# Kernel tuning notes

Hardware: AMD Instinct MI355X
Metric: run time of the kernel (lower is better)

## Reference

```python
import jax, jax.numpy as jnp
import numpy as np

N_NODES = 100000


def _sage_layer(x, src, dst, Wl, Wr, b):
    # mean-aggregate source features at destination nodes
    msgs = x[src]                                                # [E, d_in]
    agg = jax.ops.segment_sum(msgs, dst, num_segments=N_NODES)  # [N, d_in]
    cnt = jax.ops.segment_sum(jnp.ones((src.shape[0], 1), x.dtype), dst,
                              num_segments=N_NODES)             # [N, 1]
    mean = agg / jnp.maximum(cnt, 1.0)
    # PyG SAGEConv: lin_l(aggr) + lin_r(x); lin_l carries the bias
    return mean @ Wl.T + x @ Wr.T + b


def setup_inputs() -> dict:
    key = jax.random.key(0)
    ks = jax.random.split(key, 9)
    d_in, d_h, d_out, E = 128, 128, 64, 1600000
    s = 1.0 / np.sqrt(d_in)
    inp = {
        "x": jax.random.normal(ks[0], (N_NODES, d_in), jnp.float32),
        "Wl0": jax.random.normal(ks[1], (d_h, d_in), jnp.float32) * s,
        "Wr0": jax.random.normal(ks[2], (d_h, d_in), jnp.float32) * s,
        "b0": jnp.zeros((d_h,), jnp.float32),
        "Wl1": jax.random.normal(ks[3], (d_h, d_h), jnp.float32) * s,
        "Wr1": jax.random.normal(ks[4], (d_h, d_h), jnp.float32) * s,
        "b1": jnp.zeros((d_h,), jnp.float32),
        "Wl2": jax.random.normal(ks[5], (d_out, d_h), jnp.float32) * s,
        "Wr2": jax.random.normal(ks[6], (d_out, d_h), jnp.float32) * s,
        "b2": jnp.zeros((d_out,), jnp.float32),
        "edge_index": jax.random.randint(ks[7], (2, E), 0, N_NODES, jnp.int64),
    }
    return inp


def reference(x, Wl0, Wr0, b0, Wl1, Wr1, b1, Wl2, Wr2, b2, edge_index):
    src, dst = edge_index[0], edge_index[1]
    h = jax.nn.relu(_sage_layer(x, src, dst, Wl0, Wr0, b0))  # dropout = identity (eval)
    h = jax.nn.relu(_sage_layer(h, src, dst, Wl1, Wr1, b1))
    return _sage_layer(h, src, dst, Wl2, Wr2, b2)
```

## Files before the change

kernel.cpp:

```cpp
#include <hip/hip_runtime.h>

#define D 128
typedef unsigned short u16;
typedef unsigned int u32;
typedef __attribute__((ext_vector_type(8))) short short8;
typedef __attribute__((ext_vector_type(16))) float float16;

__device__ __forceinline__ u16 f2bf(float f) {
    u32 u = __builtin_bit_cast(u32, f);
    u += 0x7FFFu + ((u >> 16) & 1u);
    return (u16)(u >> 16);
}
__device__ __forceinline__ float bf2f(u16 b) {
    return __builtin_bit_cast(float, ((u32)b) << 16);
}
__device__ __forceinline__ short8 zero8() {
    short8 z;
    #pragma unroll
    for (int i = 0; i < 8; ++i) z[i] = 0;
    return z;
}


__global__ __launch_bounds__(256) void hist_kernel(const int* __restrict__ dst,
                                                   int* __restrict__ cnt, int E) {
    int e = blockIdx.x * 256 + threadIdx.x;
    if (e < E) atomicAdd(&cnt[dst[e]], 1);
}

__global__ __launch_bounds__(256) void scan1_kernel(const int* __restrict__ cnt,
        int* __restrict__ rowptr, int* __restrict__ blksum, int N) {
    __shared__ int sdata[256];
    const int base = blockIdx.x * 1024 + threadIdx.x * 4;
    int v0 = 0, v1 = 0, v2 = 0, v3 = 0;
    if (base + 3 < N) {
        int4 q = *reinterpret_cast<const int4*>(cnt + base);
        v0 = q.x; v1 = q.y; v2 = q.z; v3 = q.w;
    } else {
        if (base + 0 < N) v0 = cnt[base + 0];
        if (base + 1 < N) v1 = cnt[base + 1];
        if (base + 2 < N) v2 = cnt[base + 2];
    }
    const int t = v0 + v1 + v2 + v3;
    int val = t;
    sdata[threadIdx.x] = val;
    __syncthreads();
    for (int off = 1; off < 256; off <<= 1) {
        int other = (threadIdx.x >= off) ? sdata[threadIdx.x - off] : 0;
        __syncthreads();
        val += other;
        sdata[threadIdx.x] = val;
        __syncthreads();
    }
    const int excl = val - t;
    if (base + 0 < N) rowptr[base + 0] = excl;
    if (base + 1 < N) rowptr[base + 1] = excl + v0;
    if (base + 2 < N) rowptr[base + 2] = excl + v0 + v1;
    if (base + 3 < N) rowptr[base + 3] = excl + v0 + v1 + v2;
    if (threadIdx.x == 255) blksum[blockIdx.x] = val;
}

__global__ __launch_bounds__(256) void scan2_kernel(int* __restrict__ blksum, int nb) {
    __shared__ int s[256];
    const int t = threadIdx.x;
    const int v = (t < nb) ? blksum[t] : 0;
    int val = v;
    s[t] = val;
    __syncthreads();
    for (int off = 1; off < 256; off <<= 1) {
        int o = (t >= off) ? s[t - off] : 0;
        __syncthreads();
        val += o;
        s[t] = val;
        __syncthreads();
    }
    if (t < nb) blksum[t] = val - v;
    if (t == 255) blksum[nb] = val;
}

__global__ __launch_bounds__(256) void scan3_kernel(int* __restrict__ rowptr,
        const int* __restrict__ blksum, int N) {
    const int base = blockIdx.x * 1024 + threadIdx.x * 4;
    const int off = blksum[blockIdx.x];
    #pragma unroll
    for (int k = 0; k < 4; ++k)
        if (base + k < N) rowptr[base + k] += off;
    if (base == 0 && blockIdx.x == 0) rowptr[N] = blksum[gridDim.x];
}

__global__ __launch_bounds__(256) void invdeg_kernel(const int* __restrict__ rowptr,
        float* __restrict__ invd, int N) {
    int i = blockIdx.x * 256 + threadIdx.x;
    if (i < N) {
        int deg = rowptr[i + 1] - rowptr[i];
        invd[i] = 1.0f / (float)(deg > 1 ? deg : 1);
    }
}

__global__ __launch_bounds__(256) void fill_kernel(const int* __restrict__ src,
        const int* __restrict__ dst, const int* __restrict__ rowptr,
        int* __restrict__ fillc, int* __restrict__ colidx, int E) {
    int e = blockIdx.x * 256 + threadIdx.x;
    if (e < E) {
        int d = dst[e];
        int pos = rowptr[d] + atomicAdd(&fillc[d], 1);
        colidx[pos] = src[e];
    }
}

__global__ __launch_bounds__(256) void tobf16_kernel(const float* __restrict__ in,
        u16* __restrict__ outb, int n8) {
    int i = blockIdx.x * 256 + threadIdx.x;
    if (i >= n8) return;
    float4 a = *reinterpret_cast<const float4*>(in + (size_t)i * 8);
    float4 b = *reinterpret_cast<const float4*>(in + (size_t)i * 8 + 4);
    short8 r;
    r[0] = (short)f2bf(a.x); r[1] = (short)f2bf(a.y);
    r[2] = (short)f2bf(a.z); r[3] = (short)f2bf(a.w);
    r[4] = (short)f2bf(b.x); r[5] = (short)f2bf(b.y);
    r[6] = (short)f2bf(b.z); r[7] = (short)f2bf(b.w);
    *reinterpret_cast<short8*>(outb + (size_t)i * 8) = r;
}

__global__ __launch_bounds__(256) void gather_kernel(const u16* __restrict__ xin,
        const int* __restrict__ rowptr, const int* __restrict__ colidx,
        const float* __restrict__ invd, u16* __restrict__ outA, int N) {
    const int node = blockIdx.x * 4 + (threadIdx.x >> 6);
    if (node >= N) return;
    const int lane = threadIdx.x & 63;
    const int g = lane >> 4;
    const int r = lane & 15;
    const int beg = rowptr[node];
    const int nb = rowptr[node + 1] - beg;

    float a0 = 0.f, a1 = 0.f, a2 = 0.f, a3 = 0.f;
    float a4 = 0.f, a5 = 0.f, a6 = 0.f, a7 = 0.f;

    for (int base = 0; base < nb; base += 8) {
        const bool p0 = (base + g) < nb;
        const bool p1 = (base + 4 + g) < nb;
        uint4 v0 = make_uint4(0, 0, 0, 0), v1 = v0;
        if (p0) {
            int s0 = colidx[beg + base + g];
            v0 = *reinterpret_cast<const uint4*>(xin + (size_t)s0 * D + r * 8);
        }
        if (p1) {
            int s1 = colidx[beg + base + 4 + g];
            v1 = *reinterpret_cast<const uint4*>(xin + (size_t)s1 * D + r * 8);
        }
        a0 += bf2f((u16)v0.x) + bf2f((u16)v1.x);
        a1 += bf2f((u16)(v0.x >> 16)) + bf2f((u16)(v1.x >> 16));
        a2 += bf2f((u16)v0.y) + bf2f((u16)v1.y);
        a3 += bf2f((u16)(v0.y >> 16)) + bf2f((u16)(v1.y >> 16));
        a4 += bf2f((u16)v0.z) + bf2f((u16)v1.z);
        a5 += bf2f((u16)(v0.z >> 16)) + bf2f((u16)(v1.z >> 16));
        a6 += bf2f((u16)v0.w) + bf2f((u16)v1.w);
        a7 += bf2f((u16)(v0.w >> 16)) + bf2f((u16)(v1.w >> 16));
    }

    #pragma unroll
    for (int m = 16; m <= 32; m <<= 1) {
        a0 += __shfl_xor(a0, m, 64); a1 += __shfl_xor(a1, m, 64);
        a2 += __shfl_xor(a2, m, 64); a3 += __shfl_xor(a3, m, 64);
        a4 += __shfl_xor(a4, m, 64); a5 += __shfl_xor(a5, m, 64);
        a6 += __shfl_xor(a6, m, 64); a7 += __shfl_xor(a7, m, 64);
    }

    if (g == 0) {
        const float ic = invd[node];
        uint4 o;
        o.x = (u32)f2bf(a0 * ic) | ((u32)f2bf(a1 * ic) << 16);
        o.y = (u32)f2bf(a2 * ic) | ((u32)f2bf(a3 * ic) << 16);
        o.z = (u32)f2bf(a4 * ic) | ((u32)f2bf(a5 * ic) << 16);
        o.w = (u32)f2bf(a6 * ic) | ((u32)f2bf(a7 * ic) << 16);
        *reinterpret_cast<uint4*>(outA + (size_t)node * D + r * 8) = o;
    }
}

template<int DOUT, bool RELU, bool BF16OUT>
__global__ __launch_bounds__(256) void sage_gemm(
    const u16* __restrict__ Abf, const u16* __restrict__ Xbf,
    const float* __restrict__ Wl, const float* __restrict__ Wr,
    const float* __restrict__ bias, float* __restrict__ outf,
    u16* __restrict__ outb, int N, int nchunks)
{
    constexpr int BM = 256;
    constexpr int NKB = 4;
    constexpr int WR = (DOUT == 128) ? 2 : 4;
    constexpr int WC = 4 / WR;
    constexpr int WTM = BM / WR;
    constexpr int WTN = DOUT / WC;
    constexpr int MR = WTM / 32;
    constexpr int NC = WTN / 32;
    constexpr int LDA = 72;
    constexpr int LDW = 264;

    __shared__ u16 sW[DOUT][LDW];
    __shared__ u16 sA[2][BM][LDA];

    const int tid = threadIdx.x;
    const int lane = tid & 63;
    const int w = tid >> 6;
    const int wr = w % WR;
    const int wc = w / WR;

    for (int i = tid; i < DOUT * 64; i += 256) {
        const int c = i >> 6, q = i & 63;
        const float* sp = (q < 32) ? (Wl + (size_t)c * 128 + q * 4)
                                   : (Wr + (size_t)c * 128 + (q - 32) * 4);
        float4 wv = *reinterpret_cast<const float4*>(sp);
        u32* dp = reinterpret_cast<u32*>(&sW[c][q * 4]);
        dp[0] = (u32)f2bf(wv.x) | ((u32)f2bf(wv.y) << 16);
        dp[1] = (u32)f2bf(wv.z) | ((u32)f2bf(wv.w) << 16);
    }

    short8 rg[2][4];

    auto STAGE = [&](int kb, int m0) {
        const u16* srcb = (kb < 2) ? Abf : Xbf;
        const int koff = (kb & 1) * 64;
        #pragma unroll
        for (int p = 0; p < 2; ++p) {
            const int r = (tid >> 1) + p * 128;
            const int row = m0 + r;
            const u16* sp = srcb + (size_t)row * D + koff + (tid & 1) * 32;
            if (row < N) {
                #pragma unroll
                for (int uu = 0; uu < 4; ++uu)
                    rg[p][uu] = *reinterpret_cast<const short8*>(sp + uu * 8);
            } else {
                #pragma unroll
                for (int uu = 0; uu < 4; ++uu) rg[p][uu] = zero8();
            }
        }
    };
    auto WLDS = [&](int buf) {
        #pragma unroll
        for (int p = 0; p < 2; ++p) {
            const int r = (tid >> 1) + p * 128;
            u16* dp = &sA[buf][r][(tid & 1) * 32];
            #pragma unroll
            for (int uu = 0; uu < 4; ++uu)
                *reinterpret_cast<short8*>(dp + uu * 8) = rg[p][uu];
        }
    };

    for (int chunk = blockIdx.x; chunk < nchunks; chunk += gridDim.x) {
        const int m0 = chunk * BM;
        STAGE(0, m0);
        __syncthreads();
        WLDS(0);

        float16 acc[MR][NC];
        #pragma unroll
        for (int mi = 0; mi < MR; ++mi)
            #pragma unroll
            for (int ni = 0; ni < NC; ++ni)
                #pragma unroll
                for (int e = 0; e < 16; ++e) acc[mi][ni][e] = 0.f;

        #pragma unroll
        for (int kb = 0; kb < NKB; ++kb) {
            if (kb + 1 < NKB) STAGE(kb + 1, m0);
            __syncthreads();
            #pragma unroll
            for (int ks = 0; ks < 4; ++ks) {
                short8 af[MR], bfv[NC];
                #pragma unroll
                for (int mi = 0; mi < MR; ++mi)
                    af[mi] = *reinterpret_cast<const short8*>(
                        &sA[kb & 1][wr * WTM + mi * 32 + (lane & 31)]
                           [ks * 16 + (lane >> 5) * 8]);
                #pragma unroll
                for (int ni = 0; ni < NC; ++ni)
                    bfv[ni] = *reinterpret_cast<const short8*>(
                        &sW[wc * WTN + ni * 32 + (lane & 31)]
                           [kb * 64 + ks * 16 + (lane >> 5) * 8]);
                #pragma unroll
                for (int mi = 0; mi < MR; ++mi)
                    #pragma unroll
                    for (int ni = 0; ni < NC; ++ni)
                        acc[mi][ni] = __builtin_amdgcn_mfma_f32_32x32x16_bf16(
                            af[mi], bfv[ni], acc[mi][ni], 0, 0, 0);
            }
            if (kb + 1 < NKB) WLDS((kb + 1) & 1);
        }

        #pragma unroll
        for (int ni = 0; ni < NC; ++ni) {
            const int col = wc * WTN + ni * 32 + (lane & 31);
            const float bv = bias[col];
            #pragma unroll
            for (int mi = 0; mi < MR; ++mi) {
                #pragma unroll
                for (int e = 0; e < 16; ++e) {
                    const int row = wr * WTM + mi * 32 + 4 * (lane >> 5)
                                    + (e & 3) + 8 * (e >> 2);
                    const int grow = m0 + row;
                    if (grow < N) {
                        float v = acc[mi][ni][e] + bv;
                        if (RELU) v = fmaxf(v, 0.f);
                        if (BF16OUT) outb[(size_t)grow * DOUT + col] = f2bf(v);
                        else         outf[(size_t)grow * DOUT + col] = v;
                    }
                }
            }
        }
    }
}

extern "C" void kernel_launch(void* const* d_in, const int* in_sizes, int n_in,
                              void* d_out, int out_size, void* d_ws, size_t ws_size,
                              hipStream_t stream) {
    const float* x   = (const float*)d_in[0];
    const float* Wl0 = (const float*)d_in[1];
    const float* Wr0 = (const float*)d_in[2];
    const float* b0  = (const float*)d_in[3];
    const float* Wl1 = (const float*)d_in[4];
    const float* Wr1 = (const float*)d_in[5];
    const float* b1  = (const float*)d_in[6];
    const float* Wl2 = (const float*)d_in[7];
    const float* Wr2 = (const float*)d_in[8];
    const float* b2  = (const float*)d_in[9];
    const int* ei    = (const int*)d_in[10];

    const int E = in_sizes[10] / 2;
    const int N = in_sizes[0] / D;
    const int* src = ei;
    const int* dst = ei + E;

    u16* Xbf = (u16*)d_ws;
    u16* Abf = Xbf + (size_t)N * D;
    u16* H0  = Abf + (size_t)N * D;
    u16* H1  = H0 + (size_t)N * D;
    float* invd   = (float*)(H1 + (size_t)N * D);
    int*   cnt    = (int*)(invd + N);
    int*   rowptr = cnt + N;
    int*   blksum = rowptr + N + 8;
    int*   colidx = blksum + 512;
    float* out = (float*)d_out;

    const int NB = (N + 1023) / 1024;

    hipMemsetAsync(cnt, 0, (size_t)N * sizeof(int), stream);
    hist_kernel <<<(E + 255) / 256, 256, 0, stream>>>(dst, cnt, E);
    scan1_kernel<<<NB, 256, 0, stream>>>(cnt, rowptr, blksum, N);
    scan2_kernel<<<1, 256, 0, stream>>>(blksum, NB);
    scan3_kernel<<<NB, 256, 0, stream>>>(rowptr, blksum, N);
    invdeg_kernel<<<(N + 255) / 256, 256, 0, stream>>>(rowptr, invd, N);
    hipMemsetAsync(cnt, 0, (size_t)N * sizeof(int), stream);
    fill_kernel <<<(E + 255) / 256, 256, 0, stream>>>(src, dst, rowptr, cnt, colidx, E);

    tobf16_kernel<<<(N * D / 8 + 255) / 256, 256, 0, stream>>>(x, Xbf, N * D / 8);

    const int ggrid = (N + 3) / 4;
    const int nchunks = (N + 255) / 256;
    const int ggemm = (nchunks + 1) / 2;

    gather_kernel<<<ggrid, 256, 0, stream>>>(Xbf, rowptr, colidx, invd, Abf, N);
    sage_gemm<128, true, true><<<ggemm, 256, 0, stream>>>(
        Abf, Xbf, Wl0, Wr0, b0, nullptr, H0, N, nchunks);

    gather_kernel<<<ggrid, 256, 0, stream>>>(H0, rowptr, colidx, invd, Abf, N);
    sage_gemm<128, true, true><<<ggemm, 256, 0, stream>>>(
        Abf, H0, Wl1, Wr1, b1, nullptr, H1, N, nchunks);

    gather_kernel<<<ggrid, 256, 0, stream>>>(H1, rowptr, colidx, invd, Abf, N);
    sage_gemm<64, false, false><<<ggemm, 256, 0, stream>>>(
        Abf, H1, Wl2, Wr2, b2, out, nullptr, N, nchunks);
}
```

Baseline: 540.7 us.

## Project last layer before aggregation and reuse atomic ranks for CSR fill

```diff
diff --git a/kernel.cpp b/kernel.cpp
--- a/kernel.cpp
+++ b/kernel.cpp
@@ -23,9 +23,9 @@
 
 
 __global__ __launch_bounds__(256) void hist_kernel(const int* __restrict__ dst,
-                                                   int* __restrict__ cnt, int E) {
+        int* __restrict__ cnt, int* __restrict__ rank, int E) {
     int e = blockIdx.x * 256 + threadIdx.x;
-    if (e < E) atomicAdd(&cnt[dst[e]], 1);
+    if (e < E) rank[e] = atomicAdd(&cnt[dst[e]], 1);
 }
 
 __global__ __launch_bounds__(256) void scan1_kernel(const int* __restrict__ cnt,
@@ -99,12 +99,11 @@
 
 __global__ __launch_bounds__(256) void fill_kernel(const int* __restrict__ src,
         const int* __restrict__ dst, const int* __restrict__ rowptr,
-        int* __restrict__ fillc, int* __restrict__ colidx, int E) {
+        const int* __restrict__ rank, int* __restrict__ colidx, int E) {
     int e = blockIdx.x * 256 + threadIdx.x;
     if (e < E) {
         int d = dst[e];
-        int pos = rowptr[d] + atomicAdd(&fillc[d], 1);
-        colidx[pos] = src[e];
+        colidx[rowptr[d] + rank[e]] = src[e];
     }
 }
 
@@ -174,6 +173,52 @@
         o.z = (u32)f2bf(a4 * ic) | ((u32)f2bf(a5 * ic) << 16);
         o.w = (u32)f2bf(a6 * ic) | ((u32)f2bf(a7 * ic) << 16);
         *reinterpret_cast<uint4*>(outA + (size_t)node * D + r * 8) = o;
+    }
+}
+
+__global__ __launch_bounds__(256) void gather64_kernel(const u16* __restrict__ yin,
+        const int* __restrict__ rowptr, const int* __restrict__ colidx,
+        const float* __restrict__ invd, u16* __restrict__ outM, int N) {
+    const int node = blockIdx.x * 4 + (threadIdx.x >> 6);
+    if (node >= N) return;
+    const int lane = threadIdx.x & 63;
+    const int g = lane >> 4;
+    const int r = lane & 15;
+    const int beg = rowptr[node];
+    const int nb = rowptr[node + 1] - beg;
+
+    float a0 = 0.f, a1 = 0.f, a2 = 0.f, a3 = 0.f;
+
+    for (int base = 0; base < nb; base += 8) {
+        const bool p0 = (base + g) < nb;
+        const bool p1 = (base + 4 + g) < nb;
+        uint2 v0 = make_uint2(0, 0), v1 = v0;
+        if (p0) {
+            int s0 = colidx[beg + base + g];
+            v0 = *reinterpret_cast<const uint2*>(yin + (size_t)s0 * 64 + r * 4);
+        }
+        if (p1) {
+            int s1 = colidx[beg + base + 4 + g];
+            v1 = *reinterpret_cast<const uint2*>(yin + (size_t)s1 * 64 + r * 4);
+        }
+        a0 += bf2f((u16)v0.x) + bf2f((u16)v1.x);
+        a1 += bf2f((u16)(v0.x >> 16)) + bf2f((u16)(v1.x >> 16));
+        a2 += bf2f((u16)v0.y) + bf2f((u16)v1.y);
+        a3 += bf2f((u16)(v0.y >> 16)) + bf2f((u16)(v1.y >> 16));
+    }
+
+    #pragma unroll
+    for (int m = 16; m <= 32; m <<= 1) {
+        a0 += __shfl_xor(a0, m, 64); a1 += __shfl_xor(a1, m, 64);
+        a2 += __shfl_xor(a2, m, 64); a3 += __shfl_xor(a3, m, 64);
+    }
+
+    if (g == 0) {
+        const float ic = invd[node];
+        uint2 o;
+        o.x = (u32)f2bf(a0 * ic) | ((u32)f2bf(a1 * ic) << 16);
+        o.y = (u32)f2bf(a2 * ic) | ((u32)f2bf(a3 * ic) << 16);
+        *reinterpret_cast<uint2*>(outM + (size_t)node * 64 + r * 4) = o;
     }
 }
 
@@ -309,6 +354,129 @@
     }
 }
 
+template<bool ADDMEAN, bool BF16OUT, bool BIAS>
+__global__ __launch_bounds__(256) void lin_gemm(
+    const u16* __restrict__ In, const float* __restrict__ W,
+    const float* __restrict__ bias, const u16* __restrict__ mean2,
+    float* __restrict__ outf, u16* __restrict__ outb, int N, int nchunks)
+{
+    constexpr int DOUT = 64;
+    constexpr int BM = 256;
+    constexpr int NKB = 2;
+    constexpr int WTM = 64;
+    constexpr int MR = 2, NC = 2;
+    constexpr int LDA = 72;
+    constexpr int LDW = 136;
+
+    __shared__ u16 sW[DOUT][LDW];
+    __shared__ u16 sA[2][BM][LDA];
+
+    const int tid = threadIdx.x;
+    const int lane = tid & 63;
+    const int wr = tid >> 6;
+
+    for (int i = tid; i < DOUT * 32; i += 256) {
+        const int c = i >> 5, q = i & 31;
+        float4 wv = *reinterpret_cast<const float4*>(W + (size_t)c * 128 + q * 4);
+        u32* dp = reinterpret_cast<u32*>(&sW[c][q * 4]);
+        dp[0] = (u32)f2bf(wv.x) | ((u32)f2bf(wv.y) << 16);
+        dp[1] = (u32)f2bf(wv.z) | ((u32)f2bf(wv.w) << 16);
+    }
+
+    short8 rg[2][4];
+
+    auto STAGE = [&](int kb, int m0) {
+        const int koff = kb * 64;
+        #pragma unroll
+        for (int p = 0; p < 2; ++p) {
+            const int r = (tid >> 1) + p * 128;
+            const int row = m0 + r;
+            const u16* sp = In + (size_t)row * D + koff + (tid & 1) * 32;
+            if (row < N) {
+                #pragma unroll
+                for (int uu = 0; uu < 4; ++uu)
+                    rg[p][uu] = *reinterpret_cast<const short8*>(sp + uu * 8);
+            } else {
+                #pragma unroll
+                for (int uu = 0; uu < 4; ++uu) rg[p][uu] = zero8();
+            }
+        }
+    };
+    auto WLDS = [&](int buf) {
+        #pragma unroll
+        for (int p = 0; p < 2; ++p) {
+            const int r = (tid >> 1) + p * 128;
+            u16* dp = &sA[buf][r][(tid & 1) * 32];
+            #pragma unroll
+            for (int uu = 0; uu < 4; ++uu)
+                *reinterpret_cast<short8*>(dp + uu * 8) = rg[p][uu];
+        }
+    };
+
+    for (int chunk = blockIdx.x; chunk < nchunks; chunk += gridDim.x) {
+        const int m0 = chunk * BM;
+        STAGE(0, m0);
+        __syncthreads();
+        WLDS(0);
+
+        float16 acc[MR][NC];
+        #pragma unroll
+        for (int mi = 0; mi < MR; ++mi)
+            #pragma unroll
+            for (int ni = 0; ni < NC; ++ni)
+                #pragma unroll
+                for (int e = 0; e < 16; ++e) acc[mi][ni][e] = 0.f;
+
+        #pragma unroll
+        for (int kb = 0; kb < NKB; ++kb) {
+            if (kb + 1 < NKB) STAGE(kb + 1, m0);
+            __syncthreads();
+            #pragma unroll
+            for (int ks = 0; ks < 4; ++ks) {
+                short8 af[MR], bfv[NC];
+                #pragma unroll
+                for (int mi = 0; mi < MR; ++mi)
+                    af[mi] = *reinterpret_cast<const short8*>(
+                        &sA[kb & 1][wr * WTM + mi * 32 + (lane & 31)]
+                           [ks * 16 + (lane >> 5) * 8]);
+                #pragma unroll
+                for (int ni = 0; ni < NC; ++ni)
+                    bfv[ni] = *reinterpret_cast<const short8*>(
+                        &sW[ni * 32 + (lane & 31)]
+                           [kb * 64 + ks * 16 + (lane >> 5) * 8]);
+                #pragma unroll
+                for (int mi = 0; mi < MR; ++mi)
+                    #pragma unroll
+                    for (int ni = 0; ni < NC; ++ni)
+                        acc[mi][ni] = __builtin_amdgcn_mfma_f32_32x32x16_bf16(
+                            af[mi], bfv[ni], acc[mi][ni], 0, 0, 0);
+            }
+            if (kb + 1 < NKB) WLDS((kb + 1) & 1);
+        }
+
+        #pragma unroll
+        for (int ni = 0; ni < NC; ++ni) {
+            const int col = ni * 32 + (lane & 31);
+            const float bv = BIAS ? bias[col] : 0.f;
+            #pragma unroll
+            for (int mi = 0; mi < MR; ++mi) {
+                #pragma unroll
+                for (int e = 0; e < 16; ++e) {
+                    const int row = wr * WTM + mi * 32 + 4 * (lane >> 5)
+                                    + (e & 3) + 8 * (e >> 2);
+                    const int grow = m0 + row;
+                    if (grow < N) {
+                        float v = acc[mi][ni][e] + bv;
+                        if (ADDMEAN) v += bf2f(mean2[(size_t)grow * 64 + col]);
+                        if (BF16OUT) outb[(size_t)grow * DOUT + col] = f2bf(v);
+                        else         outf[(size_t)grow * DOUT + col] = v;
+                    }
+                }
+            }
+        }
+    }
+}
+
 extern "C" void kernel_launch(void* const* d_in, const int* in_sizes, int n_in,
                               void* d_out, int out_size, void* d_ws, size_t ws_size,
                               hipStream_t stream) {
@@ -338,18 +506,21 @@
     int*   rowptr = cnt + N;
     int*   blksum = rowptr + N + 8;
     int*   colidx = blksum + 512;
+    int*   rank   = colidx + E;
     float* out = (float*)d_out;
 
+    u16* y2    = Abf;
+    u16* mean2 = Abf + (size_t)N * 64;
+
     const int NB = (N + 1023) / 1024;
 
     hipMemsetAsync(cnt, 0, (size_t)N * sizeof(int), stream);
-    hist_kernel <<<(E + 255) / 256, 256, 0, stream>>>(dst, cnt, E);
+    hist_kernel <<<(E + 255) / 256, 256, 0, stream>>>(dst, cnt, rank, E);
     scan1_kernel<<<NB, 256, 0, stream>>>(cnt, rowptr, blksum, N);
     scan2_kernel<<<1, 256, 0, stream>>>(blksum, NB);
     scan3_kernel<<<NB, 256, 0, stream>>>(rowptr, blksum, N);
     invdeg_kernel<<<(N + 255) / 256, 256, 0, stream>>>(rowptr, invd, N);
-    hipMemsetAsync(cnt, 0, (size_t)N * sizeof(int), stream);
-    fill_kernel <<<(E + 255) / 256, 256, 0, stream>>>(src, dst, rowptr, cnt, colidx, E);
+    fill_kernel <<<(E + 255) / 256, 256, 0, stream>>>(src, dst, rowptr, rank, colidx, E);
 
     tobf16_kernel<<<(N * D / 8 + 255) / 256, 256, 0, stream>>>(x, Xbf, N * D / 8);
 
@@ -365,7 +536,9 @@
     sage_gemm<128, true, true><<<ggemm, 256, 0, stream>>>(
         Abf, H0, Wl1, Wr1, b1, nullptr, H1, N, nchunks);
 
-    gather_kernel<<<ggrid, 256, 0, stream>>>(H1, rowptr, colidx, invd, Abf, N);
-    sage_gemm<64, false, false><<<ggemm, 256, 0, stream>>>(
-        Abf, H1, Wl2, Wr2, b2, out, nullptr, N, nchunks);
-}
+    lin_gemm<false, true, false><<<ggemm, 256, 0, stream>>>(
+        H1, Wl2, nullptr, nullptr, nullptr, y2, N, nchunks);
+    gather64_kernel<<<ggrid, 256, 0, stream>>>(y2, rowptr, colidx, invd, mean2, N);
+    lin_gemm<true, false, true><<<ggemm, 256, 0, stream>>>(
+        H1, Wr2, b2, mean2, out, nullptr, N, nchunks);
+}
```

After: 518.7 us. -4.1%, faster.
